# Kernel optimization log

Measured on AMD Instinct MI355X. Metric: run time of the kernel, lower is better.

Reference implementation:

```python
import jax, jax.numpy as jnp
import numpy as np

N_NODES = 100000
N_EDGES = 1200000
N_GRAPHS = 1000
HID = 64
OUT = 4
ALPHA_FLAG = 0.03
NEG_SLOPE = 0.2


def _glorot(key, shape):
    fan_in, fan_out = shape[0], shape[-1]
    lim = (6.0 / (fan_in + fan_out)) ** 0.5
    return jax.random.uniform(key, shape, jnp.float32, -lim, lim)


def setup_inputs() -> dict:
    key = jax.random.key(0)
    ks = jax.random.split(key, 32)
    inp = {
        "x": jax.random.normal(ks[0], (N_NODES, 8), jnp.float32),
        "edge_index": jax.random.randint(ks[1], (2, N_EDGES), 0, N_NODES, jnp.int32),
        "batch": jnp.sort(jax.random.randint(ks[2], (N_NODES,), 0, N_GRAPHS, jnp.int32)),
        "climber": jax.random.normal(ks[3], (N_GRAPHS, 6), jnp.float32),
        # lin_in
        "W_in": _glorot(ks[4], (6, HID)), "b_in": jnp.zeros((HID,), jnp.float32),
        # climber_embed: LayerNorm(6) + Linear(6,64)
        "ln_g": jnp.ones((6,), jnp.float32), "ln_b": jnp.zeros((6,), jnp.float32),
        "W_c": _glorot(ks[5], (6, HID)), "b_c": jnp.zeros((HID,), jnp.float32),
        # film1 / film2: Linear(64,128)
        "Wf1": _glorot(ks[6], (HID, 2 * HID)), "bf1": jnp.zeros((2 * HID,), jnp.float32),
        "Wf2": _glorot(ks[7], (HID, 2 * HID)), "bf2": jnp.zeros((2 * HID,), jnp.float32),
        # GATConv 1 (heads=1): lin weight, att_src, att_dst, bias
        "Wg1": _glorot(ks[8], (HID, HID)), "as1": _glorot(ks[9], (HID, 1))[:, 0],
        "ad1": _glorot(ks[10], (HID, 1))[:, 0], "bg1": jnp.zeros((HID,), jnp.float32),
        # GATConv 2
        "Wg2": _glorot(ks[11], (HID, HID)), "as2": _glorot(ks[12], (HID, 1))[:, 0],
        "ad2": _glorot(ks[13], (HID, 1))[:, 0], "bg2": jnp.zeros((HID,), jnp.float32),
        # cls head
        "Wc1": _glorot(ks[14], (HID, HID)), "bc1": jnp.zeros((HID,), jnp.float32),
        "Wc2": _glorot(ks[15], (HID, OUT)), "bc2": jnp.zeros((OUT,), jnp.float32),
        # flag head
        "Wh1": _glorot(ks[16], (2, 8)), "bh1": jnp.zeros((8,), jnp.float32),
        "Wh2": _glorot(ks[17], (8, OUT)), "bh2": jnp.zeros((OUT,), jnp.float32),
    }
    return inp


def _gat(h, src, dst, W, a_src, a_dst, bias, n):
    # PyG GATConv, heads=1, concat=False, self-loops already appended.
    z = h @ W                                    # [N, H]
    e = jax.nn.leaky_relu((z @ a_src)[src] + (z @ a_dst)[dst], NEG_SLOPE)  # [E]
    m = jax.ops.segment_max(e, dst, num_segments=n)
    ex = jnp.exp(e - m[dst])
    s = jax.ops.segment_sum(ex, dst, num_segments=n)
    alpha = ex / (s[dst] + 1e-16)
    out = jax.ops.segment_sum(alpha[:, None] * z[src], dst, num_segments=n)
    return out + bias


def reference(x, edge_index, batch, climber, W_in, b_in, ln_g, ln_b, W_c, b_c,
              Wf1, bf1, Wf2, bf2, Wg1, as1, ad1, bg1, Wg2, as2, ad2, bg2,
              Wc1, bc1, Wc2, bc2, Wh1, bh1, Wh2, bh2):
    n = x.shape[0]
    # add self loops (PyG GATConv default)
    loop = jnp.arange(n, dtype=edge_index.dtype)
    src = jnp.concatenate([edge_index[0], loop])
    dst = jnp.concatenate([edge_index[1], loop])

    x_cont, flags = x[:, :6], x[:, 6:8]
    h = x_cont @ W_in + b_in

    # climber embed: LayerNorm + Linear + ReLU
    mu = jnp.mean(climber, -1, keepdims=True)
    var = jnp.var(climber, -1, keepdims=True)
    cn = (climber - mu) * jax.lax.rsqrt(var + 1e-5) * ln_g + ln_b
    c = jax.nn.relu(cn @ W_c + b_c)

    def film(h, Wf, bf):
        gb = c @ Wf + bf
        gamma, beta = jnp.split(gb, 2, axis=-1)
        return h * (1.0 + gamma[batch]) + beta[batch]

    h = film(h, Wf1, bf1)
    h = jax.nn.relu(_gat(h, src, dst, Wg1, as1, ad1, bg1, n))
    h = film(h, Wf2, bf2)
    h = jax.nn.relu(_gat(h, src, dst, Wg2, as2, ad2, bg2, n))

    # cls head (dropout inactive in eval)
    cls = jax.nn.relu(h @ Wc1 + bc1) @ Wc2 + bc2
    flag = jax.nn.relu(flags @ Wh1 + bh1) @ Wh2 + bh2
    return cls + ALPHA_FLAG * flag
```

## Files before the change

### kernel.cpp

```cpp
#include <hip/hip_runtime.h>
#include <math.h>

#define N_NODES 100000
#define N_EDGES 1200000
#define N_GRAPHS 1000
#define HID 64
#define NBUCK 256
#define NPB   391
#define BCAP  8192
#define EDGE_CHUNK 4096
#define S3_BLOCKS ((N_EDGES + EDGE_CHUNK - 1) / EDGE_CHUNK)
#define PRE_FILM_BLOCKS 125
#define PRE_BIN0 127
#define Z1_BLOCKS 256
#define LOG2E 1.4426950408889634f
#define N_TILES (N_NODES / 16)
#define AGG_BLOCKS (N_NODES / 16)

typedef _Float16 half_t;
typedef __attribute__((ext_vector_type(4))) _Float16 half4;
typedef __attribute__((ext_vector_type(8))) _Float16 half8;
typedef __attribute__((ext_vector_type(4))) float floatx4;

__global__ __launch_bounds__(1024) void k_pre(
        const float* __restrict__ climber,
        const float* __restrict__ ln_g, const float* __restrict__ ln_b,
        const float* __restrict__ W_c, const float* __restrict__ b_c,
        const float* __restrict__ Wf1, const float* __restrict__ bf1,
        const float* __restrict__ Wf2, const float* __restrict__ bf2,
        const float* __restrict__ Wg2, const float* __restrict__ Wc1,
        float* __restrict__ gb1, float* __restrict__ gb2,
        half_t* __restrict__ Wp1, half_t* __restrict__ Wp2,
        const int* __restrict__ ei, int* __restrict__ bucket_fill,
        int* __restrict__ staged) {
    int bid = blockIdx.x;
    if (bid < PRE_FILM_BLOCKS) {
        __shared__ float cl[8][64];
        int sub = threadIdx.x >> 7;
        int j   = threadIdx.x & 127;
        int g   = bid * 8 + sub;
        if (j < 64) {
            float v[6];
            float mu = 0.f;
            #pragma unroll
            for (int k = 0; k < 6; k++) { v[k] = climber[g*6+k]; mu += v[k]; }
            mu *= (1.f/6.f);
            float var = 0.f;
            #pragma unroll
            for (int k = 0; k < 6; k++) { float d = v[k]-mu; var += d*d; }
            var *= (1.f/6.f);
            float rs = rsqrtf(var + 1e-5f);
            float acc = b_c[j];
            #pragma unroll
            for (int k = 0; k < 6; k++) {
                float cn = (v[k]-mu)*rs*ln_g[k] + ln_b[k];
                acc += cn * W_c[k*64+j];
            }
            cl[sub][j] = fmaxf(acc, 0.f);
        }
        __syncthreads();
        float a1 = bf1[j], a2 = bf2[j];
        #pragma unroll 8
        for (int k = 0; k < 64; k++) {
            float ck = cl[sub][k];
            a1 += ck * Wf1[k*128+j];
            a2 += ck * Wf2[k*128+j];
        }
        gb1[g*128+j] = a1;
        gb2[g*128+j] = a2;
        return;
    }
    if (bid < PRE_BIN0) {
        const float* Wsrc = (bid == PRE_FILM_BLOCKS) ? Wg2 : Wc1;
        half_t*      Wdst = (bid == PRE_FILM_BLOCKS) ? Wp1 : Wp2;
        for (int idx = threadIdx.x; idx < 4096; idx += 1024) {
            int jj = idx & 7;
            int ko = (idx >> 3) & 1;
            int l  = (idx >> 4) & 63;
            int w  = idx >> 10;
            int c  = l & 15;
            int gg = l >> 4;
            Wdst[idx] = (half_t)Wsrc[(ko*32 + gg*8 + jj)*64 + c + 16*w];
        }
        return;
    }
    __shared__ int hist[NBUCK];
    __shared__ int cursor[NBUCK];
    for (int t = threadIdx.x; t < NBUCK; t += blockDim.x) hist[t] = 0;
    __syncthreads();
    int e0 = (bid - PRE_BIN0) * EDGE_CHUNK;
    int e1 = min(e0 + EDGE_CHUNK, N_EDGES);
    for (int e = e0 + threadIdx.x; e < e1; e += blockDim.x)
        atomicAdd(&hist[ei[N_EDGES + e] / NPB], 1);
    __syncthreads();
    if (threadIdx.x < NBUCK) {
        int hv = hist[threadIdx.x];
        int start = threadIdx.x * BCAP;
        if (hv) start += atomicAdd(&bucket_fill[threadIdx.x], hv);
        cursor[threadIdx.x] = start;
    }
    __syncthreads();
    for (int e = e0 + threadIdx.x; e < e1; e += blockDim.x) {
        int src = ei[e], dst = ei[N_EDGES + e];
        int b = dst / NPB;
        int ldst = dst - b * NPB;
        int pos = atomicAdd(&cursor[b], 1);
        staged[pos] = (ldst << 17) | src;
    }
}

__global__ __launch_bounds__(1024) void k_mid(
        const int* __restrict__ staged, const int* __restrict__ bucket_fill,
        int* __restrict__ rowptr, int* __restrict__ csr_src,
        const float* __restrict__ x, const int* __restrict__ batch,
        const float* __restrict__ W_in, const float* __restrict__ b_in,
        const float* __restrict__ gb1, const float* __restrict__ W,
        const float* __restrict__ a_src, const float* __restrict__ a_dst,
        half_t* __restrict__ z, float* __restrict__ es, float* __restrict__ ed) {
    if (blockIdx.x < NBUCK) {
        __shared__ int bb[NBUCK];
        __shared__ int ldeg[NPB];
        __shared__ int sc[512];
        __shared__ int cursor[NPB];
        int b = blockIdx.x;
        if (threadIdx.x < NBUCK) bb[threadIdx.x] = bucket_fill[threadIdx.x];
        __syncthreads();
        for (int off = 1; off < NBUCK; off <<= 1) {
            int u = 0;
            if (threadIdx.x < NBUCK && threadIdx.x >= off) u = bb[threadIdx.x - off];
            __syncthreads();
            if (threadIdx.x < NBUCK) bb[threadIdx.x] += u;
            __syncthreads();
        }
        int bbase = (b == 0) ? 0 : bb[b-1];
        int bcnt  = bb[b] - bbase;
        const int* st = staged + b * BCAP;
        int n0 = b * NPB;
        int n1 = min(n0 + NPB, N_NODES);
        int nn = n1 - n0;
        for (int t = threadIdx.x; t < NPB; t += blockDim.x) ldeg[t] = 0;
        __syncthreads();
        for (int k = threadIdx.x; k < bcnt; k += blockDim.x)
            atomicAdd(&ldeg[st[k] >> 17], 1);
        __syncthreads();
        if (threadIdx.x < 512) sc[threadIdx.x] = (threadIdx.x < nn) ? ldeg[threadIdx.x] : 0;
        __syncthreads();
        for (int off = 1; off < 512; off <<= 1) {
            int u = 0;
            if (threadIdx.x < 512 && threadIdx.x >= off) u = sc[threadIdx.x - off];
            __syncthreads();
            if (threadIdx.x < 512) sc[threadIdx.x] += u;
            __syncthreads();
        }
        if (threadIdx.x < nn) {
            int pre = sc[threadIdx.x] - ldeg[threadIdx.x];
            rowptr[n0 + threadIdx.x] = bbase + pre;
            cursor[threadIdx.x] = bbase + pre;
        }
        if (b == 0 && threadIdx.x == 0) rowptr[N_NODES] = bb[NBUCK-1];
        __syncthreads();
        for (int k = threadIdx.x; k < bcnt; k += blockDim.x) {
            int v = st[k];
            int pos = atomicAdd(&cursor[v >> 17], 1);
            csr_src[pos] = v & 0x1FFFF;
        }
        return;
    }
    __shared__ float Wi[384];
    __shared__ float bi[64];
    __shared__ __align__(16) half_t zl[16][1024];
    for (int idx = threadIdx.x; idx < 384; idx += 1024) Wi[idx] = W_in[idx];
    if (threadIdx.x < 64) bi[threadIdx.x] = b_in[threadIdx.x];
    int wave = threadIdx.x >> 6;
    int l    = threadIdx.x & 63;
    int c    = l & 15;
    int g    = l >> 4;
    half8 Bf[2][4];
    #pragma unroll
    for (int ko = 0; ko < 2; ko++) {
        #pragma unroll
        for (int nt = 0; nt < 4; nt++) {
            half8 bvec;
            #pragma unroll
            for (int j = 0; j < 8; j++)
                bvec[j] = (half_t)W[(ko*32 + g*8 + j)*64 + c + 16*nt];
            Bf[ko][nt] = bvec;
        }
    }
    float as4[4], ad4[4];
    #pragma unroll
    for (int nt = 0; nt < 4; nt++) {
        as4[nt] = a_src[c + 16*nt] * LOG2E;
        ad4[nt] = a_dst[c + 16*nt] * LOG2E;
    }
    __syncthreads();
    int nWaves = Z1_BLOCKS * 16;
    int wid = (blockIdx.x - NBUCK) * 16 + wave;
    half_t* zw = zl[wave];
    const float4* x4p = (const float4*)x;
    for (int t = wid; t < N_TILES; t += nWaves) {
        int m0 = t * 16;
        int i = m0 + c;
        float4 xa = x4p[i*2];
        float4 xb = x4p[i*2 + 1];
        float xv[6] = {xa.x, xa.y, xa.z, xa.w, xb.x, xb.y};
        int bg_ = batch[i];
        half8 A[2];
        #pragma unroll
        for (int s = 0; s < 2; s++) {
            int bk = s*32 + g*8;
            float acc[8];
            #pragma unroll
            for (int j = 0; j < 8; j++) acc[j] = bi[bk + j];
            #pragma unroll
            for (int kk = 0; kk < 6; kk++) {
                float xk = xv[kk];
                float4 w0 = *(const float4*)&Wi[kk*64 + bk];
                float4 w1 = *(const float4*)&Wi[kk*64 + bk + 4];
                acc[0] += xk*w0.x; acc[1] += xk*w0.y;
                acc[2] += xk*w0.z; acc[3] += xk*w0.w;
                acc[4] += xk*w1.x; acc[5] += xk*w1.y;
                acc[6] += xk*w1.z; acc[7] += xk*w1.w;
            }
            const float4* gbv = (const float4*)(gb1 + bg_*128);
            float4 ga0 = gbv[bk/4],      ga1 = gbv[bk/4 + 1];
            float4 be0 = gbv[16 + bk/4], be1 = gbv[16 + bk/4 + 1];
            half8 hv;
            hv[0] = (half_t)(acc[0]*(1.f+ga0.x) + be0.x);
            hv[1] = (half_t)(acc[1]*(1.f+ga0.y) + be0.y);
            hv[2] = (half_t)(acc[2]*(1.f+ga0.z) + be0.z);
            hv[3] = (half_t)(acc[3]*(1.f+ga0.w) + be0.w);
            hv[4] = (half_t)(acc[4]*(1.f+ga1.x) + be1.x);
            hv[5] = (half_t)(acc[5]*(1.f+ga1.y) + be1.y);
            hv[6] = (half_t)(acc[6]*(1.f+ga1.z) + be1.z);
            hv[7] = (half_t)(acc[7]*(1.f+ga1.w) + be1.w);
            A[s] = hv;
        }
        floatx4 D[4];
        #pragma unroll
        for (int nt = 0; nt < 4; nt++) {
            floatx4 acc = {0.f, 0.f, 0.f, 0.f};
            acc = __builtin_amdgcn_mfma_f32_16x16x32_f16(A[0], Bf[0][nt], acc, 0, 0, 0);
            acc = __builtin_amdgcn_mfma_f32_16x16x32_f16(A[1], Bf[1][nt], acc, 0, 0, 0);
            D[nt] = acc;
        }
        #pragma unroll
        for (int r = 0; r < 4; r++) {
            float ps = D[0][r]*as4[0] + D[1][r]*as4[1] + D[2][r]*as4[2] + D[3][r]*as4[3];
            float pd = D[0][r]*ad4[0] + D[1][r]*ad4[1] + D[2][r]*ad4[2] + D[3][r]*ad4[3];
            #pragma unroll
            for (int off = 1; off < 16; off <<= 1) {
                ps += __shfl_xor(ps, off, 16);
                pd += __shfl_xor(pd, off, 16);
            }
            if (c == 0) {
                es[m0 + g*4 + r] = ps;
                ed[m0 + g*4 + r] = pd;
            }
        }
        #pragma unroll
        for (int nt = 0; nt < 4; nt++) {
            #pragma unroll
            for (int r = 0; r < 4; r++)
                zw[(g*4 + r)*64 + c + 16*nt] = (half_t)D[nt][r];
        }
        __asm__ __volatile__("s_waitcnt lgkmcnt(0)" ::: "memory");
        const half8* zr = (const half8*)zw;
        half8 v0 = zr[l*2];
        half8 v1 = zr[l*2 + 1];
        half8* zo = (half8*)(z + (size_t)m0 * 64);
        zo[l*2]     = v0;
        zo[l*2 + 1] = v1;
        __asm__ __volatile__("s_waitcnt lgkmcnt(0)" ::: "memory");
    }
}

__device__ __forceinline__ float4 h4_to_f4(half4 h) {
    float4 f;
    f.x = (float)h.x; f.y = (float)h.y; f.z = (float)h.z; f.w = (float)h.w;
    return f;
}

template<int MODE>
__global__ __launch_bounds__(256) void k_agg_f(
        const int* __restrict__ rowptr, const int* __restrict__ csr_src,
        const float* __restrict__ es, const float* __restrict__ ed,
        const half_t* __restrict__ z, const float* __restrict__ bg,
        const int* __restrict__ batch, const float* __restrict__ gb,
        const half_t* __restrict__ Wp,
        const float* __restrict__ av_s, const float* __restrict__ av_d,
        half_t* __restrict__ zout, float* __restrict__ es_o, float* __restrict__ ed_o,
        const float* __restrict__ x,
        const float* __restrict__ bc1, const float* __restrict__ Wc2,
        const float* __restrict__ bc2,
        const float* __restrict__ Wh1, const float* __restrict__ bh1,
        const float* __restrict__ Wh2, const float* __restrict__ bh2,
        float* __restrict__ out) {
    __shared__ __align__(16) half_t h_l[1024];
    __shared__ __align__(16) half_t zl16[1024];
    __shared__ float red[4][16][4];
    int tidb = threadIdx.x;
    int il = tidb >> 4;
    int sl = tidb & 15;
    int m0 = blockIdx.x * 16;
    int i = m0 + il;

    int l    = tidb & 63;
    int wave = tidb >> 6;
    int c    = l & 15;
    int g    = l >> 4;
    const half8* wp = (const half8*)(Wp + ((size_t)tidb << 4));
    half8 Bf0 = wp[0];
    half8 Bf1 = wp[1];
    float as_w = 0.f, ad_w = 0.f, bc1w = 0.f;
    float4 w2w = {0.f, 0.f, 0.f, 0.f};
    if (MODE == 1) {
        as_w = av_s[c + 16*wave] * LOG2E;
        ad_w = av_d[c + 16*wave] * LOG2E;
    } else {
        bc1w = bc1[c + 16*wave];
        w2w  = ((const float4*)Wc2)[c + 16*wave];
    }

    int beg = rowptr[i], end = rowptr[i+1];
    int deg = end - beg;
    float edi = ed[i];

    int svA = 0, svB = 0;
    if (sl < deg)      svA = csr_src[beg + sl];
    if (16 + sl < deg) svB = csr_src[beg + 16 + sl];

    const half4* z4 = (const half4*)z;
    int aP[16];
    #pragma unroll
    for (int j = 0; j < 16; j++) aP[j] = __shfl(svA, j, 16);
    half4 qP[16];
    #pragma unroll
    for (int j = 0; j < 16; j++) qP[j] = z4[aP[j]*16 + sl];
    float4 zi = h4_to_f4(z4[i*16 + sl]);
    float esA = es[svA];
    float esB = es[svB];
    float e_self = es[i] + edi;
    e_self = fmaxf(e_self, 0.2f * e_self);
    float vA = esA + edi, vB = esB + edi;
    float exA = (sl < deg)      ? exp2f(fmaxf(vA, 0.2f * vA)) : 0.f;
    float exB = (16 + sl < deg) ? exp2f(fmaxf(vB, 0.2f * vB)) : 0.f;

    float s = exA + exB;
    #pragma unroll
    for (int off = 1; off < 16; off <<= 1)
        s += __shfl_xor(s, off, 16);
    float ex = exp2f(e_self);
    s += ex;

    float4 acc = {ex*zi.x, ex*zi.y, ex*zi.z, ex*zi.w};

    #pragma unroll
    for (int j = 0; j < 16; j++) {
        float e = __shfl(exA, j, 16);
        float4 r = h4_to_f4(qP[j]);
        acc.x += e*r.x; acc.y += e*r.y;
        acc.z += e*r.z; acc.w += e*r.w;
    }

    if (deg > 16) {
        int lim = (deg < 32) ? deg : 32;
        int k = 16;
        for (; k + 8 <= lim; k += 8) {
            int a[8]; float e[8];
            #pragma unroll
            for (int j = 0; j < 8; j++) {
                a[j] = __shfl(svB, k-16+j, 16);
                e[j] = __shfl(exB, k-16+j, 16);
            }
            half4 q[8];
            #pragma unroll
            for (int j = 0; j < 8; j++) q[j] = z4[a[j]*16 + sl];
            #pragma unroll
            for (int j = 0; j < 8; j++) {
                float4 r = h4_to_f4(q[j]);
                acc.x += e[j]*r.x; acc.y += e[j]*r.y;
                acc.z += e[j]*r.z; acc.w += e[j]*r.w;
            }
        }
        for (; k + 4 <= lim; k += 4) {
            int a[4]; float e[4];
            #pragma unroll
            for (int j = 0; j < 4; j++) {
                a[j] = __shfl(svB, k-16+j, 16);
                e[j] = __shfl(exB, k-16+j, 16);
            }
            half4 q[4];
            #pragma unroll
            for (int j = 0; j < 4; j++) q[j] = z4[a[j]*16 + sl];
            #pragma unroll
            for (int j = 0; j < 4; j++) {
                float4 r = h4_to_f4(q[j]);
                acc.x += e[j]*r.x; acc.y += e[j]*r.y;
                acc.z += e[j]*r.z; acc.w += e[j]*r.w;
            }
        }
        for (; k < lim; k++) {
            int a = __shfl(svB, k-16, 16);
            float e2 = __shfl(exB, k-16, 16);
            float4 zr = h4_to_f4(z4[a*16 + sl]);
            acc.x += e2*zr.x; acc.y += e2*zr.y; acc.z += e2*zr.z; acc.w += e2*zr.w;
        }
        for (int kk = beg + 32; kk < end; kk++) {
            int sv = csr_src[kk];
            float v = es[sv] + edi;
            float e2 = exp2f(fmaxf(v, 0.2f * v));
            s += e2;
            float4 zr = h4_to_f4(z4[sv*16 + sl]);
            acc.x += e2*zr.x; acc.y += e2*zr.y; acc.z += e2*zr.z; acc.w += e2*zr.w;
        }
    }
    float inv = 1.f / (s + 1e-16f);
    float4 bg4 = ((const float4*)bg)[sl];
    float4 o;
    o.x = fmaxf(acc.x*inv + bg4.x, 0.f);
    o.y = fmaxf(acc.y*inv + bg4.y, 0.f);
    o.z = fmaxf(acc.z*inv + bg4.z, 0.f);
    o.w = fmaxf(acc.w*inv + bg4.w, 0.f);
    if (MODE == 1) {
        int gidx = batch[i];
        const float4* gb4 = (const float4*)gb;
        float4 ga = gb4[gidx*32 + sl];
        float4 be = gb4[gidx*32 + 16 + sl];
        o.x = o.x*(1.f+ga.x) + be.x;
        o.y = o.y*(1.f+ga.y) + be.y;
        o.z = o.z*(1.f+ga.z) + be.z;
        o.w = o.w*(1.f+ga.w) + be.w;
    }
    half4 hv;
    hv.x = (half_t)o.x; hv.y = (half_t)o.y; hv.z = (half_t)o.z; hv.w = (half_t)o.w;
    *(half4*)((char*)h_l + il*128 + ((sl*8) ^ ((il & 7) << 4))) = hv;

    __syncthreads();
    half8 A0 = *(const half8*)((const char*)h_l + c*128 + ((g*16)      ^ ((c & 7) << 4)));
    half8 A1 = *(const half8*)((const char*)h_l + c*128 + ((64 + g*16) ^ ((c & 7) << 4)));
    floatx4 D = {0.f, 0.f, 0.f, 0.f};
    D = __builtin_amdgcn_mfma_f32_16x16x32_f16(A0, Bf0, D, 0, 0, 0);
    D = __builtin_amdgcn_mfma_f32_16x16x32_f16(A1, Bf1, D, 0, 0, 0);
    if (MODE == 1) {
        #pragma unroll
        for (int r = 0; r < 4; r++) {
            float ps = D[r]*as_w, pd = D[r]*ad_w;
            #pragma unroll
            for (int off = 1; off < 16; off <<= 1) {
                ps += __shfl_xor(ps, off, 16);
                pd += __shfl_xor(pd, off, 16);
            }
            if (c == 0) {
                red[wave][g*4 + r][0] = ps;
                red[wave][g*4 + r][1] = pd;
            }
            zl16[(g*4 + r)*64 + c + 16*wave] = (half_t)D[r];
        }
        __syncthreads();
        if (tidb < 16) {
            es_o[m0 + tidb] = red[0][tidb][0] + red[1][tidb][0] + red[2][tidb][0] + red[3][tidb][0];
            ed_o[m0 + tidb] = red[0][tidb][1] + red[1][tidb][1] + red[2][tidb][1] + red[3][tidb][1];
        }
        if (tidb < 128)
            ((half8*)(zout + (size_t)m0 * 64))[tidb] = ((const half8*)zl16)[tidb];
    } else {
        #pragma unroll
        for (int r = 0; r < 4; r++) {
            float tv = fmaxf(D[r] + bc1w, 0.f);
            float px = tv*w2w.x, py = tv*w2w.y, pz = tv*w2w.z, pw = tv*w2w.w;
            #pragma unroll
            for (int off = 1; off < 16; off <<= 1) {
                px += __shfl_xor(px, off, 16);
                py += __shfl_xor(py, off, 16);
                pz += __shfl_xor(pz, off, 16);
                pw += __shfl_xor(pw, off, 16);
            }
            if (c == 0) {
                red[wave][g*4 + r][0] = px;
                red[wave][g*4 + r][1] = py;
                red[wave][g*4 + r][2] = pz;
                red[wave][g*4 + r][3] = pw;
            }
        }
        __syncthreads();
        if (tidb < 16) {
            int m = m0 + tidb;
            float p0 = red[0][tidb][0] + red[1][tidb][0] + red[2][tidb][0] + red[3][tidb][0] + bc2[0];
            float p1 = red[0][tidb][1] + red[1][tidb][1] + red[2][tidb][1] + red[3][tidb][1] + bc2[1];
            float p2 = red[0][tidb][2] + red[1][tidb][2] + red[2][tidb][2] + red[3][tidb][2] + bc2[2];
            float p3 = red[0][tidb][3] + red[1][tidb][3] + red[2][tidb][3] + red[3][tidb][3] + bc2[3];
            float f0 = x[m*8+6], f1 = x[m*8+7];
            float t8[8];
            #pragma unroll
            for (int q = 0; q < 8; q++)
                t8[q] = fmaxf(f0*Wh1[q] + f1*Wh1[8+q] + bh1[q], 0.f);
            float fl[4];
            #pragma unroll
            for (int q = 0; q < 4; q++) {
                float a = bh2[q];
                #pragma unroll
                for (int rr = 0; rr < 8; rr++) a += t8[rr]*Wh2[rr*4+q];
                fl[q] = a;
            }
            float4 ov;
            ov.x = p0 + 0.03f*fl[0];
            ov.y = p1 + 0.03f*fl[1];
            ov.z = p2 + 0.03f*fl[2];
            ov.w = p3 + 0.03f*fl[3];
            ((float4*)out)[m] = ov;
        }
    }
}

extern "C" void kernel_launch(void* const* d_in, const int* in_sizes, int n_in,
                              void* d_out, int out_size, void* d_ws, size_t ws_size,
                              hipStream_t stream) {
    const float* x       = (const float*)d_in[0];
    const int*   ei      = (const int*)  d_in[1];
    const int*   batch   = (const int*)  d_in[2];
    const float* climber = (const float*)d_in[3];
    const float* W_in    = (const float*)d_in[4];
    const float* b_in    = (const float*)d_in[5];
    const float* ln_g    = (const float*)d_in[6];
    const float* ln_b    = (const float*)d_in[7];
    const float* W_c     = (const float*)d_in[8];
    const float* b_c     = (const float*)d_in[9];
    const float* Wf1     = (const float*)d_in[10];
    const float* bf1     = (const float*)d_in[11];
    const float* Wf2     = (const float*)d_in[12];
    const float* bf2     = (const float*)d_in[13];
    const float* Wg1     = (const float*)d_in[14];
    const float* as1     = (const float*)d_in[15];
    const float* ad1     = (const float*)d_in[16];
    const float* bg1     = (const float*)d_in[17];
    const float* Wg2     = (const float*)d_in[18];
    const float* as2     = (const float*)d_in[19];
    const float* ad2     = (const float*)d_in[20];
    const float* bg2     = (const float*)d_in[21];
    const float* Wc1     = (const float*)d_in[22];
    const float* bc1     = (const float*)d_in[23];
    const float* Wc2     = (const float*)d_in[24];
    const float* bc2     = (const float*)d_in[25];
    const float* Wh1     = (const float*)d_in[26];
    const float* bh1     = (const float*)d_in[27];
    const float* Wh2     = (const float*)d_in[28];
    const float* bh2     = (const float*)d_in[29];
    float* out = (float*)d_out;
    float* ws  = (float*)d_ws;

    float*  gb1         = ws;
    float*  gb2         = gb1 + 128000;
    half_t* Wp1         = (half_t*)(gb2 + 128000);
    half_t* Wp2         = Wp1 + 4096;
    half_t* zA          = Wp2 + 4096;
    half_t* zB          = zA + 6400000;
    float*  es1         = (float*)(zB + 6400000);
    float*  ed1         = es1 + N_NODES;
    float*  es2         = ed1 + N_NODES;
    float*  ed2         = es2 + N_NODES;
    int*    rowptr      = (int*)(ed2 + N_NODES);
    int*    csr_src     = rowptr + N_NODES + 1;
    int*    bucket_fill = csr_src + N_EDGES;
    int*    staged      = bucket_fill + NBUCK;

    hipMemsetAsync(bucket_fill, 0, NBUCK * sizeof(int), stream);

    k_pre<<<PRE_BIN0 + S3_BLOCKS, 1024, 0, stream>>>(climber, ln_g, ln_b, W_c, b_c,
                                                     Wf1, bf1, Wf2, bf2, Wg2, Wc1,
                                                     gb1, gb2, Wp1, Wp2,
                                                     ei, bucket_fill, staged);

    k_mid<<<NBUCK + Z1_BLOCKS, 1024, 0, stream>>>(staged, bucket_fill, rowptr, csr_src,
                                                  x, batch, W_in, b_in, gb1, Wg1,
                                                  as1, ad1, zA, es1, ed1);

    k_agg_f<1><<<AGG_BLOCKS, 256, 0, stream>>>(rowptr, csr_src, es1, ed1, zA, bg1,
                                               batch, gb2, Wp1, as2, ad2,
                                               zB, es2, ed2,
                                               nullptr, nullptr, nullptr, nullptr,
                                               nullptr, nullptr, nullptr, nullptr,
                                               nullptr);

    k_agg_f<2><<<AGG_BLOCKS, 256, 0, stream>>>(rowptr, csr_src, es2, ed2, zB, bg2,
                                               batch, nullptr, Wp2, nullptr, nullptr,
                                               nullptr, nullptr, nullptr,
                                               x, bc1, Wc2, bc2, Wh1, bh1, Wh2, bh2,
                                               out);
}
```

Before: 237.3 us.

## Aggregate 32 nodes per block with 8 lanes per node and half8 gathers

The fused aggregation kernel now gives each block 32 destination nodes instead of 16, with 8 threads per node each gathering a 16-byte half8 slice of the neighbour feature row. The projection that follows runs two MFMA row tiles per block, and the shared buffers are doubled to match. The aim is fewer, wider memory transactions per gathered row and half as many blocks, spreading the per-block weight-fragment loads over more nodes. In exchange each thread holds more registers (16 half8 prefetches plus 8 accumulators), which may lower occupancy.

```diff
diff --git a/kernel.cpp b/kernel.cpp
--- a/kernel.cpp
+++ b/kernel.cpp
@@ -15,7 +15,7 @@
 #define Z1_BLOCKS 256
 #define LOG2E 1.4426950408889634f
 #define N_TILES (N_NODES / 16)
-#define AGG_BLOCKS (N_NODES / 16)
+#define AGG_BLOCKS (N_NODES / 32)
 
 typedef _Float16 half_t;
 typedef __attribute__((ext_vector_type(4))) _Float16 half4;
@@ -275,12 +275,6 @@
     }
 }
 
-__device__ __forceinline__ float4 h4_to_f4(half4 h) {
-    float4 f;
-    f.x = (float)h.x; f.y = (float)h.y; f.z = (float)h.z; f.w = (float)h.w;
-    return f;
-}
-
 template<int MODE>
 __global__ __launch_bounds__(256) void k_agg_f(
         const int* __restrict__ rowptr, const int* __restrict__ csr_src,
@@ -296,13 +290,13 @@
         const float* __restrict__ Wh1, const float* __restrict__ bh1,
         const float* __restrict__ Wh2, const float* __restrict__ bh2,
         float* __restrict__ out) {
-    __shared__ __align__(16) half_t h_l[1024];
-    __shared__ __align__(16) half_t zl16[1024];
-    __shared__ float red[4][16][4];
+    __shared__ __align__(16) half_t h_l[2048];
+    __shared__ __align__(16) half_t zl32[2048];
+    __shared__ float red[4][32][4];
     int tidb = threadIdx.x;
-    int il = tidb >> 4;
-    int sl = tidb & 15;
-    int m0 = blockIdx.x * 16;
+    int il = tidb >> 3;
+    int q  = tidb & 7;
+    int m0 = blockIdx.x * 32;
     int i = m0 + il;
 
     int l    = tidb & 63;
@@ -326,165 +320,187 @@
     int deg = end - beg;
     float edi = ed[i];
 
-    int svA = 0, svB = 0;
-    if (sl < deg)      svA = csr_src[beg + sl];
-    if (16 + sl < deg) svB = csr_src[beg + 16 + sl];
-
-    const half4* z4 = (const half4*)z;
-    int aP[16];
-    #pragma unroll
-    for (int j = 0; j < 16; j++) aP[j] = __shfl(svA, j, 16);
-    half4 qP[16];
-    #pragma unroll
-    for (int j = 0; j < 16; j++) qP[j] = z4[aP[j]*16 + sl];
-    float4 zi = h4_to_f4(z4[i*16 + sl]);
-    float esA = es[svA];
-    float esB = es[svB];
-    float e_self = es[i] + edi;
-    e_self = fmaxf(e_self, 0.2f * e_self);
-    float vA = esA + edi, vB = esB + edi;
-    float exA = (sl < deg)      ? exp2f(fmaxf(vA, 0.2f * vA)) : 0.f;
-    float exB = (16 + sl < deg) ? exp2f(fmaxf(vB, 0.2f * vB)) : 0.f;
-
-    float s = exA + exB;
-    #pragma unroll
-    for (int off = 1; off < 16; off <<= 1)
-        s += __shfl_xor(s, off, 16);
-    float ex = exp2f(e_self);
+    int idA[2];
+    #pragma unroll
+    for (int j = 0; j < 2; j++) {
+        int k = j*8 + q;
+        idA[j] = (k < deg) ? csr_src[beg + k] : 0;
+    }
+    bool big = (deg > 16);
+    int idB[2] = {0, 0};
+    if (big) {
+        #pragma unroll
+        for (int j = 0; j < 2; j++) {
+            int k = 16 + j*8 + q;
+            idB[j] = (k < deg) ? csr_src[beg + k] : 0;
+        }
+    }
+
+    int sv16[16];
+    #pragma unroll
+    for (int k = 0; k < 16; k++) sv16[k] = __shfl(idA[k >> 3], k & 7, 8);
+    half8 qP[16];
+    #pragma unroll
+    for (int k = 0; k < 16; k++)
+        qP[k] = *(const half8*)(z + (size_t)sv16[k]*64 + q*8);
+    half8 zself = *(const half8*)(z + (size_t)i*64 + q*8);
+
+    float exA[2], exB[2] = {0.f, 0.f};
+    #pragma unroll
+    for (int j = 0; j < 2; j++) {
+        float v = es[idA[j]] + edi;
+        v = fmaxf(v, 0.2f * v);
+        exA[j] = (j*8 + q < deg) ? exp2f(v) : 0.f;
+    }
+    if (big) {
+        #pragma unroll
+        for (int j = 0; j < 2; j++) {
+            float v = es[idB[j]] + edi;
+            v = fmaxf(v, 0.2f * v);
+            exB[j] = (16 + j*8 + q < deg) ? exp2f(v) : 0.f;
+        }
+    }
+    float s = exA[0] + exA[1] + exB[0] + exB[1];
+    s += __shfl_xor(s, 1, 8);
+    s += __shfl_xor(s, 2, 8);
+    s += __shfl_xor(s, 4, 8);
+    float vs = es[i] + edi;
+    vs = fmaxf(vs, 0.2f * vs);
+    float ex = exp2f(vs);
     s += ex;
 
-    float4 acc = {ex*zi.x, ex*zi.y, ex*zi.z, ex*zi.w};
-
-    #pragma unroll
-    for (int j = 0; j < 16; j++) {
-        float e = __shfl(exA, j, 16);
-        float4 r = h4_to_f4(qP[j]);
-        acc.x += e*r.x; acc.y += e*r.y;
-        acc.z += e*r.z; acc.w += e*r.w;
-    }
-
-    if (deg > 16) {
-        int lim = (deg < 32) ? deg : 32;
-        int k = 16;
-        for (; k + 8 <= lim; k += 8) {
-            int a[8]; float e[8];
-            #pragma unroll
-            for (int j = 0; j < 8; j++) {
-                a[j] = __shfl(svB, k-16+j, 16);
-                e[j] = __shfl(exB, k-16+j, 16);
-            }
-            half4 q[8];
-            #pragma unroll
-            for (int j = 0; j < 8; j++) q[j] = z4[a[j]*16 + sl];
-            #pragma unroll
-            for (int j = 0; j < 8; j++) {
-                float4 r = h4_to_f4(q[j]);
-                acc.x += e[j]*r.x; acc.y += e[j]*r.y;
-                acc.z += e[j]*r.z; acc.w += e[j]*r.w;
-            }
-        }
-        for (; k + 4 <= lim; k += 4) {
-            int a[4]; float e[4];
-            #pragma unroll
-            for (int j = 0; j < 4; j++) {
-                a[j] = __shfl(svB, k-16+j, 16);
-                e[j] = __shfl(exB, k-16+j, 16);
-            }
-            half4 q[4];
-            #pragma unroll
-            for (int j = 0; j < 4; j++) q[j] = z4[a[j]*16 + sl];
-            #pragma unroll
-            for (int j = 0; j < 4; j++) {
-                float4 r = h4_to_f4(q[j]);
-                acc.x += e[j]*r.x; acc.y += e[j]*r.y;
-                acc.z += e[j]*r.z; acc.w += e[j]*r.w;
-            }
-        }
-        for (; k < lim; k++) {
-            int a = __shfl(svB, k-16, 16);
-            float e2 = __shfl(exB, k-16, 16);
-            float4 zr = h4_to_f4(z4[a*16 + sl]);
-            acc.x += e2*zr.x; acc.y += e2*zr.y; acc.z += e2*zr.z; acc.w += e2*zr.w;
+    float acc[8];
+    #pragma unroll
+    for (int t = 0; t < 8; t++) acc[t] = ex * (float)zself[t];
+
+    #pragma unroll
+    for (int k = 0; k < 16; k++) {
+        float e = __shfl(exA[k >> 3], k & 7, 8);
+        half8 r = qP[k];
+        #pragma unroll
+        for (int t = 0; t < 8; t++) acc[t] += e * (float)r[t];
+    }
+
+    if (big) {
+        #pragma unroll
+        for (int h = 0; h < 2; h++) {
+            int svh[8];
+            #pragma unroll
+            for (int k = 0; k < 8; k++) svh[k] = __shfl(idB[h], k, 8);
+            half8 qh[8];
+            #pragma unroll
+            for (int k = 0; k < 8; k++)
+                qh[k] = *(const half8*)(z + (size_t)svh[k]*64 + q*8);
+            #pragma unroll
+            for (int k = 0; k < 8; k++) {
+                float e = __shfl(exB[h], k, 8);
+                half8 r = qh[k];
+                #pragma unroll
+                for (int t = 0; t < 8; t++) acc[t] += e * (float)r[t];
+            }
         }
         for (int kk = beg + 32; kk < end; kk++) {
             int sv = csr_src[kk];
             float v = es[sv] + edi;
             float e2 = exp2f(fmaxf(v, 0.2f * v));
             s += e2;
-            float4 zr = h4_to_f4(z4[sv*16 + sl]);
-            acc.x += e2*zr.x; acc.y += e2*zr.y; acc.z += e2*zr.z; acc.w += e2*zr.w;
-        }
-    }
+            half8 zr = *(const half8*)(z + (size_t)sv*64 + q*8);
+            #pragma unroll
+            for (int t = 0; t < 8; t++) acc[t] += e2 * (float)zr[t];
+        }
+    }
+
     float inv = 1.f / (s + 1e-16f);
-    float4 bg4 = ((const float4*)bg)[sl];
-    float4 o;
-    o.x = fmaxf(acc.x*inv + bg4.x, 0.f);
-    o.y = fmaxf(acc.y*inv + bg4.y, 0.f);
-    o.z = fmaxf(acc.z*inv + bg4.z, 0.f);
-    o.w = fmaxf(acc.w*inv + bg4.w, 0.f);
+    const float4* bgv = (const float4*)bg;
+    float4 b0 = bgv[q*2], b1 = bgv[q*2 + 1];
+    float o[8];
+    o[0] = fmaxf(acc[0]*inv + b0.x, 0.f);
+    o[1] = fmaxf(acc[1]*inv + b0.y, 0.f);
+    o[2] = fmaxf(acc[2]*inv + b0.z, 0.f);
+    o[3] = fmaxf(acc[3]*inv + b0.w, 0.f);
+    o[4] = fmaxf(acc[4]*inv + b1.x, 0.f);
+    o[5] = fmaxf(acc[5]*inv + b1.y, 0.f);
+    o[6] = fmaxf(acc[6]*inv + b1.z, 0.f);
+    o[7] = fmaxf(acc[7]*inv + b1.w, 0.f);
     if (MODE == 1) {
         int gidx = batch[i];
-        const float4* gb4 = (const float4*)gb;
-        float4 ga = gb4[gidx*32 + sl];
-        float4 be = gb4[gidx*32 + 16 + sl];
-        o.x = o.x*(1.f+ga.x) + be.x;
-        o.y = o.y*(1.f+ga.y) + be.y;
-        o.z = o.z*(1.f+ga.z) + be.z;
-        o.w = o.w*(1.f+ga.w) + be.w;
-    }
-    half4 hv;
-    hv.x = (half_t)o.x; hv.y = (half_t)o.y; hv.z = (half_t)o.z; hv.w = (half_t)o.w;
-    *(half4*)((char*)h_l + il*128 + ((sl*8) ^ ((il & 7) << 4))) = hv;
+        const float4* gb4 = (const float4*)(gb + gidx*128);
+        float4 ga0 = gb4[q*2],      ga1 = gb4[q*2 + 1];
+        float4 be0 = gb4[16 + q*2], be1 = gb4[16 + q*2 + 1];
+        o[0] = o[0]*(1.f+ga0.x) + be0.x;
+        o[1] = o[1]*(1.f+ga0.y) + be0.y;
+        o[2] = o[2]*(1.f+ga0.z) + be0.z;
+        o[3] = o[3]*(1.f+ga0.w) + be0.w;
+        o[4] = o[4]*(1.f+ga1.x) + be1.x;
+        o[5] = o[5]*(1.f+ga1.y) + be1.y;
+        o[6] = o[6]*(1.f+ga1.z) + be1.z;
+        o[7] = o[7]*(1.f+ga1.w) + be1.w;
+    }
+    half8 hv;
+    #pragma unroll
+    for (int t = 0; t < 8; t++) hv[t] = (half_t)o[t];
+    *(half8*)((char*)h_l + il*128 + ((q*16) ^ ((il & 7) << 4))) = hv;
 
     __syncthreads();
-    half8 A0 = *(const half8*)((const char*)h_l + c*128 + ((g*16)      ^ ((c & 7) << 4)));
-    half8 A1 = *(const half8*)((const char*)h_l + c*128 + ((64 + g*16) ^ ((c & 7) << 4)));
-    floatx4 D = {0.f, 0.f, 0.f, 0.f};
-    D = __builtin_amdgcn_mfma_f32_16x16x32_f16(A0, Bf0, D, 0, 0, 0);
-    D = __builtin_amdgcn_mfma_f32_16x16x32_f16(A1, Bf1, D, 0, 0, 0);
+    floatx4 D[2];
+    #pragma unroll
+    for (int mt = 0; mt < 2; mt++) {
+        int row = mt*16 + c;
+        half8 A0 = *(const half8*)((const char*)h_l + row*128 + ((g*16)      ^ ((row & 7) << 4)));
+        half8 A1 = *(const half8*)((const char*)h_l + row*128 + ((64 + g*16) ^ ((row & 7) << 4)));
+        floatx4 a = {0.f, 0.f, 0.f, 0.f};
+        a = __builtin_amdgcn_mfma_f32_16x16x32_f16(A0, Bf0, a, 0, 0, 0);
+        a = __builtin_amdgcn_mfma_f32_16x16x32_f16(A1, Bf1, a, 0, 0, 0);
+        D[mt] = a;
+    }
     if (MODE == 1) {
         #pragma unroll
-        for (int r = 0; r < 4; r++) {
-            float ps = D[r]*as_w, pd = D[r]*ad_w;
-            #pragma unroll
-            for (int off = 1; off < 16; off <<= 1) {
-                ps += __shfl_xor(ps, off, 16);
-                pd += __shfl_xor(pd, off, 16);
-            }
-            if (c == 0) {
-                red[wave][g*4 + r][0] = ps;
-                red[wave][g*4 + r][1] = pd;
-            }
-            zl16[(g*4 + r)*64 + c + 16*wave] = (half_t)D[r];
-        }
-        __syncthreads();
-        if (tidb < 16) {
+        for (int mt = 0; mt < 2; mt++) {
+            #pragma unroll
+            for (int r = 0; r < 4; r++) {
+                float ps = D[mt][r]*as_w, pd = D[mt][r]*ad_w;
+                #pragma unroll
+                for (int off = 1; off < 16; off <<= 1) {
+                    ps += __shfl_xor(ps, off, 16);
+                    pd += __shfl_xor(pd, off, 16);
+                }
+                if (c == 0) {
+                    red[wave][mt*16 + g*4 + r][0] = ps;
+                    red[wave][mt*16 + g*4 + r][1] = pd;
+                }
+                zl32[(mt*16 + g*4 + r)*64 + c + 16*wave] = (half_t)D[mt][r];
+            }
+        }
+        __syncthreads();
+        if (tidb < 32) {
             es_o[m0 + tidb] = red[0][tidb][0] + red[1][tidb][0] + red[2][tidb][0] + red[3][tidb][0];
             ed_o[m0 + tidb] = red[0][tidb][1] + red[1][tidb][1] + red[2][tidb][1] + red[3][tidb][1];
         }
-        if (tidb < 128)
-            ((half8*)(zout + (size_t)m0 * 64))[tidb] = ((const half8*)zl16)[tidb];
+        ((half8*)(zout + (size_t)m0 * 64))[tidb] = ((const half8*)zl32)[tidb];
     } else {
         #pragma unroll
-        for (int r = 0; r < 4; r++) {
-            float tv = fmaxf(D[r] + bc1w, 0.f);
-            float px = tv*w2w.x, py = tv*w2w.y, pz = tv*w2w.z, pw = tv*w2w.w;
-            #pragma unroll
-            for (int off = 1; off < 16; off <<= 1) {
-                px += __shfl_xor(px, off, 16);
-                py += __shfl_xor(py, off, 16);
-                pz += __shfl_xor(pz, off, 16);
-                pw += __shfl_xor(pw, off, 16);
-            }
-            if (c == 0) {
-                red[wave][g*4 + r][0] = px;
-                red[wave][g*4 + r][1] = py;
-                red[wave][g*4 + r][2] = pz;
-                red[wave][g*4 + r][3] = pw;
-            }
-        }
-        __syncthreads();
-        if (tidb < 16) {
+        for (int mt = 0; mt < 2; mt++) {
+            #pragma unroll
+            for (int r = 0; r < 4; r++) {
+                float tv = fmaxf(D[mt][r] + bc1w, 0.f);
+                float px = tv*w2w.x, py = tv*w2w.y, pz = tv*w2w.z, pw = tv*w2w.w;
+                #pragma unroll
+                for (int off = 1; off < 16; off <<= 1) {
+                    px += __shfl_xor(px, off, 16);
+                    py += __shfl_xor(py, off, 16);
+                    pz += __shfl_xor(pz, off, 16);
+                    pw += __shfl_xor(pw, off, 16);
+                }
+                if (c == 0) {
+                    red[wave][mt*16 + g*4 + r][0] = px;
+                    red[wave][mt*16 + g*4 + r][1] = py;
+                    red[wave][mt*16 + g*4 + r][2] = pz;
+                    red[wave][mt*16 + g*4 + r][3] = pw;
+                }
+            }
+        }
+        __syncthreads();
+        if (tidb < 32) {
             int m = m0 + tidb;
             float p0 = red[0][tidb][0] + red[1][tidb][0] + red[2][tidb][0] + red[3][tidb][0] + bc2[0];
             float p1 = red[0][tidb][1] + red[1][tidb][1] + red[2][tidb][1] + red[3][tidb][1] + bc2[1];
@@ -493,15 +509,15 @@
             float f0 = x[m*8+6], f1 = x[m*8+7];
             float t8[8];
             #pragma unroll
-            for (int q = 0; q < 8; q++)
-                t8[q] = fmaxf(f0*Wh1[q] + f1*Wh1[8+q] + bh1[q], 0.f);
+            for (int qq = 0; qq < 8; qq++)
+                t8[qq] = fmaxf(f0*Wh1[qq] + f1*Wh1[8+qq] + bh1[qq], 0.f);
             float fl[4];
             #pragma unroll
-            for (int q = 0; q < 4; q++) {
-                float a = bh2[q];
+            for (int qq = 0; qq < 4; qq++) {
+                float a = bh2[qq];
                 #pragma unroll
-                for (int rr = 0; rr < 8; rr++) a += t8[rr]*Wh2[rr*4+q];
-                fl[q] = a;
+                for (int rr = 0; rr < 8; rr++) a += t8[rr]*Wh2[rr*4+qq];
+                fl[qq] = a;
             }
             float4 ov;
             ov.x = p0 + 0.03f*fl[0];
```

After: 245.8 us. +3.6%, slower.

## Reschedule preprocessing kernels: fold memset, overlap binning with z1 GEMM

Applied to the files above, without the earlier changes.

Restructures the preprocessing pipeline. The bucket_fill memset is folded into a small FiLM/weight-pack kernel. The edge binning pass now runs in the same launch as the first-layer z projection, so the two overlap. The bucket-to-CSR conversion moves to its own 512-thread kernel. The binning loop also keeps each thread's edges in registers so the edge indices are read only once. In exchange there is one extra kernel launch, and the z1 GEMM now runs alongside binning instead of alongside the CSR build.

```diff
diff --git a/kernel.cpp b/kernel.cpp
--- a/kernel.cpp
+++ b/kernel.cpp
@@ -10,8 +10,6 @@
 #define BCAP  8192
 #define EDGE_CHUNK 4096
 #define S3_BLOCKS ((N_EDGES + EDGE_CHUNK - 1) / EDGE_CHUNK)
-#define PRE_FILM_BLOCKS 125
-#define PRE_BIN0 127
 #define Z1_BLOCKS 256
 #define LOG2E 1.4426950408889634f
 #define N_TILES (N_NODES / 16)
@@ -22,7 +20,7 @@
 typedef __attribute__((ext_vector_type(8))) _Float16 half8;
 typedef __attribute__((ext_vector_type(4))) float floatx4;
 
-__global__ __launch_bounds__(1024) void k_pre(
+__global__ __launch_bounds__(1024) void k_film(
         const float* __restrict__ climber,
         const float* __restrict__ ln_g, const float* __restrict__ ln_b,
         const float* __restrict__ W_c, const float* __restrict__ b_c,
@@ -31,48 +29,12 @@
         const float* __restrict__ Wg2, const float* __restrict__ Wc1,
         float* __restrict__ gb1, float* __restrict__ gb2,
         half_t* __restrict__ Wp1, half_t* __restrict__ Wp2,
-        const int* __restrict__ ei, int* __restrict__ bucket_fill,
-        int* __restrict__ staged) {
+        int* __restrict__ bucket_fill) {
     int bid = blockIdx.x;
-    if (bid < PRE_FILM_BLOCKS) {
-        __shared__ float cl[8][64];
-        int sub = threadIdx.x >> 7;
-        int j   = threadIdx.x & 127;
-        int g   = bid * 8 + sub;
-        if (j < 64) {
-            float v[6];
-            float mu = 0.f;
-            #pragma unroll
-            for (int k = 0; k < 6; k++) { v[k] = climber[g*6+k]; mu += v[k]; }
-            mu *= (1.f/6.f);
-            float var = 0.f;
-            #pragma unroll
-            for (int k = 0; k < 6; k++) { float d = v[k]-mu; var += d*d; }
-            var *= (1.f/6.f);
-            float rs = rsqrtf(var + 1e-5f);
-            float acc = b_c[j];
-            #pragma unroll
-            for (int k = 0; k < 6; k++) {
-                float cn = (v[k]-mu)*rs*ln_g[k] + ln_b[k];
-                acc += cn * W_c[k*64+j];
-            }
-            cl[sub][j] = fmaxf(acc, 0.f);
-        }
-        __syncthreads();
-        float a1 = bf1[j], a2 = bf2[j];
-        #pragma unroll 8
-        for (int k = 0; k < 64; k++) {
-            float ck = cl[sub][k];
-            a1 += ck * Wf1[k*128+j];
-            a2 += ck * Wf2[k*128+j];
-        }
-        gb1[g*128+j] = a1;
-        gb2[g*128+j] = a2;
-        return;
-    }
-    if (bid < PRE_BIN0) {
-        const float* Wsrc = (bid == PRE_FILM_BLOCKS) ? Wg2 : Wc1;
-        half_t*      Wdst = (bid == PRE_FILM_BLOCKS) ? Wp1 : Wp2;
+    if (bid == 0 && threadIdx.x < NBUCK) bucket_fill[threadIdx.x] = 0;
+    if (bid >= 125) {
+        const float* Wsrc = (bid == 125) ? Wg2 : Wc1;
+        half_t*      Wdst = (bid == 125) ? Wp1 : Wp2;
         for (int idx = threadIdx.x; idx < 4096; idx += 1024) {
             int jj = idx & 7;
             int ko = (idx >> 3) & 1;
@@ -84,85 +46,85 @@
         }
         return;
     }
-    __shared__ int hist[NBUCK];
-    __shared__ int cursor[NBUCK];
-    for (int t = threadIdx.x; t < NBUCK; t += blockDim.x) hist[t] = 0;
-    __syncthreads();
-    int e0 = (bid - PRE_BIN0) * EDGE_CHUNK;
-    int e1 = min(e0 + EDGE_CHUNK, N_EDGES);
-    for (int e = e0 + threadIdx.x; e < e1; e += blockDim.x)
-        atomicAdd(&hist[ei[N_EDGES + e] / NPB], 1);
-    __syncthreads();
-    if (threadIdx.x < NBUCK) {
-        int hv = hist[threadIdx.x];
-        int start = threadIdx.x * BCAP;
-        if (hv) start += atomicAdd(&bucket_fill[threadIdx.x], hv);
-        cursor[threadIdx.x] = start;
-    }
-    __syncthreads();
-    for (int e = e0 + threadIdx.x; e < e1; e += blockDim.x) {
-        int src = ei[e], dst = ei[N_EDGES + e];
-        int b = dst / NPB;
-        int ldst = dst - b * NPB;
-        int pos = atomicAdd(&cursor[b], 1);
-        staged[pos] = (ldst << 17) | src;
-    }
+    __shared__ float cl[8][64];
+    int sub = threadIdx.x >> 7;
+    int j   = threadIdx.x & 127;
+    int g   = bid * 8 + sub;
+    if (j < 64) {
+        float v[6];
+        float mu = 0.f;
+        #pragma unroll
+        for (int k = 0; k < 6; k++) { v[k] = climber[g*6+k]; mu += v[k]; }
+        mu *= (1.f/6.f);
+        float var = 0.f;
+        #pragma unroll
+        for (int k = 0; k < 6; k++) { float d = v[k]-mu; var += d*d; }
+        var *= (1.f/6.f);
+        float rs = rsqrtf(var + 1e-5f);
+        float acc = b_c[j];
+        #pragma unroll
+        for (int k = 0; k < 6; k++) {
+            float cn = (v[k]-mu)*rs*ln_g[k] + ln_b[k];
+            acc += cn * W_c[k*64+j];
+        }
+        cl[sub][j] = fmaxf(acc, 0.f);
+    }
+    __syncthreads();
+    float a1 = bf1[j], a2 = bf2[j];
+    #pragma unroll 8
+    for (int k = 0; k < 64; k++) {
+        float ck = cl[sub][k];
+        a1 += ck * Wf1[k*128+j];
+        a2 += ck * Wf2[k*128+j];
+    }
+    gb1[g*128+j] = a1;
+    gb2[g*128+j] = a2;
 }
 
-__global__ __launch_bounds__(1024) void k_mid(
-        const int* __restrict__ staged, const int* __restrict__ bucket_fill,
-        int* __restrict__ rowptr, int* __restrict__ csr_src,
+__global__ __launch_bounds__(1024) void k_pre2(
+        const int* __restrict__ ei, int* __restrict__ bucket_fill,
+        int* __restrict__ staged,
         const float* __restrict__ x, const int* __restrict__ batch,
         const float* __restrict__ W_in, const float* __restrict__ b_in,
         const float* __restrict__ gb1, const float* __restrict__ W,
         const float* __restrict__ a_src, const float* __restrict__ a_dst,
         half_t* __restrict__ z, float* __restrict__ es, float* __restrict__ ed) {
-    if (blockIdx.x < NBUCK) {
-        __shared__ int bb[NBUCK];
-        __shared__ int ldeg[NPB];
-        __shared__ int sc[512];
-        __shared__ int cursor[NPB];
-        int b = blockIdx.x;
-        if (threadIdx.x < NBUCK) bb[threadIdx.x] = bucket_fill[threadIdx.x];
-        __syncthreads();
-        for (int off = 1; off < NBUCK; off <<= 1) {
-            int u = 0;
-            if (threadIdx.x < NBUCK && threadIdx.x >= off) u = bb[threadIdx.x - off];
-            __syncthreads();
-            if (threadIdx.x < NBUCK) bb[threadIdx.x] += u;
-            __syncthreads();
-        }
-        int bbase = (b == 0) ? 0 : bb[b-1];
-        int bcnt  = bb[b] - bbase;
-        const int* st = staged + b * BCAP;
-        int n0 = b * NPB;
-        int n1 = min(n0 + NPB, N_NODES);
-        int nn = n1 - n0;
-        for (int t = threadIdx.x; t < NPB; t += blockDim.x) ldeg[t] = 0;
-        __syncthreads();
-        for (int k = threadIdx.x; k < bcnt; k += blockDim.x)
-            atomicAdd(&ldeg[st[k] >> 17], 1);
-        __syncthreads();
-        if (threadIdx.x < 512) sc[threadIdx.x] = (threadIdx.x < nn) ? ldeg[threadIdx.x] : 0;
-        __syncthreads();
-        for (int off = 1; off < 512; off <<= 1) {
-            int u = 0;
-            if (threadIdx.x < 512 && threadIdx.x >= off) u = sc[threadIdx.x - off];
-            __syncthreads();
-            if (threadIdx.x < 512) sc[threadIdx.x] += u;
-            __syncthreads();
-        }
-        if (threadIdx.x < nn) {
-            int pre = sc[threadIdx.x] - ldeg[threadIdx.x];
-            rowptr[n0 + threadIdx.x] = bbase + pre;
-            cursor[threadIdx.x] = bbase + pre;
-        }
-        if (b == 0 && threadIdx.x == 0) rowptr[N_NODES] = bb[NBUCK-1];
-        __syncthreads();
-        for (int k = threadIdx.x; k < bcnt; k += blockDim.x) {
-            int v = st[k];
-            int pos = atomicAdd(&cursor[v >> 17], 1);
-            csr_src[pos] = v & 0x1FFFF;
+    if (blockIdx.x < S3_BLOCKS) {
+        __shared__ int hist[NBUCK];
+        __shared__ int cursor[NBUCK];
+        for (int t = threadIdx.x; t < NBUCK; t += 1024) hist[t] = 0;
+        __syncthreads();
+        int e0 = blockIdx.x * EDGE_CHUNK;
+        int n  = min(EDGE_CHUNK, N_EDGES - e0);
+        int srcs[4], ldsts[4], bks[4];
+        #pragma unroll
+        for (int j = 0; j < 4; j++) {
+            int idx = threadIdx.x + j*1024;
+            bks[j] = -1;
+            if (idx < n) {
+                int e = e0 + idx;
+                srcs[j] = ei[e];
+                int dst = ei[N_EDGES + e];
+                int b = dst / NPB;
+                bks[j] = b;
+                ldsts[j] = dst - b * NPB;
+                atomicAdd(&hist[b], 1);
+            }
+        }
+        __syncthreads();
+        if (threadIdx.x < NBUCK) {
+            int hv = hist[threadIdx.x];
+            int start = threadIdx.x * BCAP;
+            if (hv) start += atomicAdd(&bucket_fill[threadIdx.x], hv);
+            cursor[threadIdx.x] = start;
+        }
+        __syncthreads();
+        #pragma unroll
+        for (int j = 0; j < 4; j++) {
+            if (bks[j] >= 0) {
+                int pos = atomicAdd(&cursor[bks[j]], 1);
+                staged[pos] = (ldsts[j] << 17) | srcs[j];
+            }
         }
         return;
     }
@@ -195,7 +157,7 @@
     }
     __syncthreads();
     int nWaves = Z1_BLOCKS * 16;
-    int wid = (blockIdx.x - NBUCK) * 16 + wave;
+    int wid = (blockIdx.x - S3_BLOCKS) * 16 + wave;
     half_t* zw = zl[wave];
     const float4* x4p = (const float4*)x;
     for (int t = wid; t < N_TILES; t += nWaves) {
@@ -272,6 +234,57 @@
         zo[l*2]     = v0;
         zo[l*2 + 1] = v1;
         __asm__ __volatile__("s_waitcnt lgkmcnt(0)" ::: "memory");
+    }
+}
+
+__global__ __launch_bounds__(512) void k_bcsr(
+        const int* __restrict__ staged, const int* __restrict__ bucket_fill,
+        int* __restrict__ rowptr, int* __restrict__ csr_src) {
+    __shared__ int bb[NBUCK];
+    __shared__ int ldeg[NPB];
+    __shared__ int sc[512];
+    __shared__ int cursor[NPB];
+    int b = blockIdx.x;
+    if (threadIdx.x < NBUCK) bb[threadIdx.x] = bucket_fill[threadIdx.x];
+    __syncthreads();
+    for (int off = 1; off < NBUCK; off <<= 1) {
+        int u = 0;
+        if (threadIdx.x < NBUCK && threadIdx.x >= off) u = bb[threadIdx.x - off];
+        __syncthreads();
+        if (threadIdx.x < NBUCK) bb[threadIdx.x] += u;
+        __syncthreads();
+    }
+    int bbase = (b == 0) ? 0 : bb[b-1];
+    int bcnt  = bb[b] - bbase;
+    const int* st = staged + b * BCAP;
+    int n0 = b * NPB;
+    int n1 = min(n0 + NPB, N_NODES);
+    int nn = n1 - n0;
+    for (int t = threadIdx.x; t < NPB; t += 512) ldeg[t] = 0;
+    __syncthreads();
+    for (int k = threadIdx.x; k < bcnt; k += 512)
+        atomicAdd(&ldeg[st[k] >> 17], 1);
+    __syncthreads();
+    sc[threadIdx.x] = (threadIdx.x < nn) ? ldeg[threadIdx.x] : 0;
+    __syncthreads();
+    for (int off = 1; off < 512; off <<= 1) {
+        int u = 0;
+        if (threadIdx.x >= off) u = sc[threadIdx.x - off];
+        __syncthreads();
+        sc[threadIdx.x] += u;
+        __syncthreads();
+    }
+    if (threadIdx.x < nn) {
+        int pre = sc[threadIdx.x] - ldeg[threadIdx.x];
+        rowptr[n0 + threadIdx.x] = bbase + pre;
+        cursor[threadIdx.x] = bbase + pre;
+    }
+    if (b == 0 && threadIdx.x == 0) rowptr[N_NODES] = bb[NBUCK-1];
+    __syncthreads();
+    for (int k = threadIdx.x; k < bcnt; k += 512) {
+        int v = st[k];
+        int pos = atomicAdd(&cursor[v >> 17], 1);
+        csr_src[pos] = v & 0x1FFFF;
     }
 }
 
@@ -564,16 +577,15 @@
     int*    bucket_fill = csr_src + N_EDGES;
     int*    staged      = bucket_fill + NBUCK;
 
-    hipMemsetAsync(bucket_fill, 0, NBUCK * sizeof(int), stream);
-
-    k_pre<<<PRE_BIN0 + S3_BLOCKS, 1024, 0, stream>>>(climber, ln_g, ln_b, W_c, b_c,
-                                                     Wf1, bf1, Wf2, bf2, Wg2, Wc1,
-                                                     gb1, gb2, Wp1, Wp2,
-                                                     ei, bucket_fill, staged);
-
-    k_mid<<<NBUCK + Z1_BLOCKS, 1024, 0, stream>>>(staged, bucket_fill, rowptr, csr_src,
-                                                  x, batch, W_in, b_in, gb1, Wg1,
-                                                  as1, ad1, zA, es1, ed1);
+    k_film<<<127, 1024, 0, stream>>>(climber, ln_g, ln_b, W_c, b_c,
+                                     Wf1, bf1, Wf2, bf2, Wg2, Wc1,
+                                     gb1, gb2, Wp1, Wp2, bucket_fill);
+
+    k_pre2<<<S3_BLOCKS + Z1_BLOCKS, 1024, 0, stream>>>(ei, bucket_fill, staged,
+                                                       x, batch, W_in, b_in, gb1, Wg1,
+                                                       as1, ad1, zA, es1, ed1);
+
+    k_bcsr<<<NBUCK, 512, 0, stream>>>(staged, bucket_fill, rowptr, csr_src);
 
     k_agg_f<1><<<AGG_BLOCKS, 256, 0, stream>>>(rowptr, csr_src, es1, ed1, zA, bg1,
                                                batch, gb2, Wp1, as2, ad2,
```

Measured after the change: 233.1 us (median of 2 runs). Within noise of the previous version (-1.8%).
